# Optimization experiments

Hardware: AMD Instinct MI355X
Metric: run time of the kernel (lower is better)

Reference implementation:

```python
import jax, jax.numpy as jnp
import numpy as np

EPS = 1e-5

def headwise_linear(x, w):
    # x: [B,S,D], w: [NH, DH_out, DH_in] block-diagonal linear per head
    B, S, D = x.shape
    NH, O, DH = w.shape
    xh = x.reshape(B, S, NH, DH)
    return jnp.einsum('bshd,hod->bsho', xh, w).reshape(B, S, NH * O)

def setup_inputs() -> dict:
    key = jax.random.key(0)
    ks = jax.random.split(key, 10)
    B, S, D, NH, K = 8, 4096, 768, 4, 4
    DH = D // NH
    small = (2.0 / (5.0 * D)) ** 0.5  # small_init scale
    return {
        'x': jax.random.normal(ks[0], (B, S, D), jnp.float32),
        'conv_w': jax.random.normal(ks[1], (D, 1, K), jnp.float32) * (1.0 / K ** 0.5),
        'conv_b': jnp.zeros((D,), jnp.float32),
        'w_f': jax.random.normal(ks[2], (NH, DH, DH), jnp.float32) * small,
        'w_i': jax.random.normal(ks[3], (NH, DH, DH), jnp.float32) * small,
        'w_z': jax.random.normal(ks[4], (NH, DH, DH), jnp.float32) * small,
        'w_o': jax.random.normal(ks[5], (NH, DH, DH), jnp.float32) * small,
        'r_kernel': jax.random.normal(ks[6], (NH, DH, 4, DH), jnp.float32) * (1.0 / DH ** 0.5),
        'r_bias': jnp.zeros((4, NH, DH), jnp.float32),
        'gn_weight': jnp.ones((D,), jnp.float32),
    }

def reference(x, conv_w, conv_b, w_f, w_i, w_z, w_o, r_kernel, r_bias, gn_weight):
    B, S, D = x.shape
    NH, DH = r_kernel.shape[0], r_kernel.shape[1]
    K = conv_w.shape[-1]
    # --- causal depthwise conv1d + SiLU ---
    xt = jnp.transpose(x, (0, 2, 1))  # [B,D,S]
    xc = jax.lax.conv_general_dilated(xt, conv_w, (1,), [(K - 1, 0)],
                                      feature_group_count=D)
    x_conv = jax.nn.silu(jnp.transpose(xc + conv_b[None, :, None], (0, 2, 1)))
    # --- headwise gate projections (note: original code feeds fgate->i, igate->f) ---
    gi = headwise_linear(x_conv, w_f)
    gf = headwise_linear(x_conv, w_i)
    gz = headwise_linear(x, w_z)
    go = headwise_linear(x, w_o)
    Wx = jnp.stack([gi, gf, gz, go], axis=2).reshape(B, S, 4, NH, DH)
    Wx = jnp.transpose(Wx, (1, 0, 2, 3, 4))  # [S,B,4,NH,DH]
    # --- sLSTM recurrent scan with exponential gating + stabilizer m ---
    def step(carry, wx_t):
        y, c, n, m = carry  # each [B,NH,DH]
        Ry = jnp.einsum('bhd,hdge->bghe', y, r_kernel)  # [B,4,NH,DH]
        raw = wx_t + Ry + r_bias[None]
        iraw, fraw, zraw, oraw = raw[:, 0], raw[:, 1], raw[:, 2], raw[:, 3]
        logfplusm = m + jax.nn.log_sigmoid(fraw)
        mnew = jnp.maximum(iraw, logfplusm)
        igate = jnp.exp(iraw - mnew)
        fgate = jnp.exp(logfplusm - mnew)
        cnew = fgate * c + igate * jnp.tanh(zraw)
        nnew = fgate * n + igate
        ynew = jax.nn.sigmoid(oraw) * cnew / nnew
        return (ynew, cnew, nnew, mnew), ynew
    init = tuple(jnp.zeros((B, NH, DH), x.dtype) for _ in range(4))
    _, ys = jax.lax.scan(step, init, Wx)  # [S,B,NH,DH]
    y = jnp.transpose(ys, (1, 2, 0, 3))  # [B,NH,S,DH]
    # --- multi-head layer norm (group norm with NH groups over DH) ---
    mean = y.mean(-1, keepdims=True)
    var = y.var(-1, keepdims=True)
    yn = (y - mean) * jax.lax.rsqrt(var + EPS)
    yn = yn * gn_weight.reshape(1, NH, 1, DH)
    return jnp.transpose(yn, (0, 2, 1, 3)).reshape(B, S, NH * DH)
```

## Files before the change

kernel.cpp:

```cpp
#include <hip/hip_runtime.h>
#include <hip/hip_bf16.h>
#include <math.h>

#define B_ 8
#define S_ 4096
#define D_ 768
#define NH_ 4
#define DH_ 192
#define NTOT_ 768

typedef __attribute__((ext_vector_type(8))) short short8;
typedef __attribute__((ext_vector_type(4))) float floatx4;
typedef __attribute__((ext_vector_type(4))) short short4v;
typedef __attribute__((ext_vector_type(4))) unsigned int uint4v;
typedef _Float16 f16;

__device__ __forceinline__ short f2bs(float f) {
  union { float f; unsigned u; } v; v.f = f;
  unsigned r = v.u + 0x7FFFu + ((v.u >> 16) & 1u);
  return (short)(r >> 16);
}
__device__ __forceinline__ float bs2f(unsigned short s) {
  union { unsigned u; float f; } v; v.u = ((unsigned)s) << 16;
  return v.f;
}
__device__ __forceinline__ unsigned packh2(float lo, float hi) {
  union { f16 h[2]; unsigned u; } x;
  x.h[0] = (f16)lo; x.h[1] = (f16)hi;
  return x.u;
}

__device__ __forceinline__ float DOT2(unsigned r, unsigned y, float acc) {
  asm("v_dot2_f32_f16 %0, %1, %2, %0" : "+v"(acc) : "v"(r), "v"(y));
  return acc;
}

template<int CTRL>
__device__ __forceinline__ float qperm(float x) {
  return __int_as_float(__builtin_amdgcn_mov_dpp(__float_as_int(x), CTRL, 0xf, 0xf, true));
}

__global__ __launch_bounds__(256) void wconv_kernel(
    const float* __restrict__ wf, const float* __restrict__ wi,
    const float* __restrict__ wz, const float* __restrict__ wo,
    short* __restrict__ Wbf)
{
  int idx = blockIdx.x * 256 + threadIdx.x;
  int hg = idx / (DH_ * DH_);
  int r  = idx % (DH_ * DH_);
  int h = hg >> 2, g = hg & 3;
  const float* W = (g == 0) ? wf : (g == 1) ? wi : (g == 2) ? wz : wo;
  Wbf[idx] = f2bs(W[(size_t)h * DH_ * DH_ + r]);
}

__global__ __launch_bounds__(256) void conv_silu_kernel(
    const float* __restrict__ x, const float* __restrict__ cw, const float* __restrict__ cb,
    short* __restrict__ xb, short* __restrict__ xcb)
{
  const int b  = blockIdx.x / (S_ / 64);
  const int s0 = (blockIdx.x % (S_ / 64)) * 64;
  const int tid = threadIdx.x;
  float wv[3][4], bias[3], win[3][3];
  for (int j = 0; j < 3; ++j) {
    int d = tid + j * 256;
    for (int k = 0; k < 4; ++k) wv[j][k] = cw[d * 4 + k];
    bias[j] = cb[d];
    for (int p = 0; p < 3; ++p) {
      int s = s0 - 3 + p;
      win[j][p] = (s >= 0) ? x[((size_t)b * S_ + s) * D_ + d] : 0.f;
    }
  }
  for (int i = 0; i < 64; ++i) {
    size_t base = ((size_t)b * S_ + (s0 + i)) * D_;
    for (int j = 0; j < 3; ++j) {
      int d = tid + j * 256;
      float xc = x[base + d];
      float a = bias[j] + win[j][0] * wv[j][0] + win[j][1] * wv[j][1]
                        + win[j][2] * wv[j][2] + xc * wv[j][3];
      float sv = a / (1.f + __expf(-a));
      xb[base + d]  = f2bs(xc);
      xcb[base + d] = f2bs(sv);
      win[j][0] = win[j][1]; win[j][1] = win[j][2]; win[j][2] = xc;
    }
  }
}

__global__ __launch_bounds__(256) void proj_kernel(
    const short* __restrict__ xb, const short* __restrict__ xcb,
    const short* __restrict__ Wbf, const float* __restrict__ rb,
    short* __restrict__ P)
{
  const int hg = blockIdx.y;
  const int h = hg >> 2, g = hg & 3;
  const short* A  = (g < 2) ? xcb : xb;
  const short* Wb = Wbf + (size_t)hg * (DH_ * DH_);
  const int tid = threadIdx.x, w = tid >> 6, l = tid & 63;
  const int l15 = l & 15, lg = l >> 4;
  const int R0 = blockIdx.x * 256 + w * 64;

  float rbv[12];
#pragma unroll
  for (int nt = 0; nt < 12; ++nt)
    rbv[nt] = rb[(g * NH_ + h) * DH_ + l15 + nt * 16];

  for (int mp = 0; mp < 2; ++mp) {
    const int rb0 = R0 + mp * 32;
    floatx4 acc[2][12];
    for (int u = 0; u < 2; ++u)
      for (int nt = 0; nt < 12; ++nt) acc[u][nt] = (floatx4){0.f, 0.f, 0.f, 0.f};
    const short* Ar = A + (size_t)(rb0 + l15) * D_ + h * DH_ + lg * 8;
    const short* Bp = Wb + l15 * DH_ + lg * 8;
    for (int kk = 0; kk < 6; ++kk) {
      short8 a0 = *(const short8*)(Ar + kk * 32);
      short8 a1 = *(const short8*)(Ar + (size_t)16 * D_ + kk * 32);
      for (int nt = 0; nt < 12; ++nt) {
        short8 bf = *(const short8*)(Bp + nt * 16 * DH_ + kk * 32);
        acc[0][nt] = __builtin_amdgcn_mfma_f32_16x16x32_bf16(a0, bf, acc[0][nt], 0, 0, 0);
        acc[1][nt] = __builtin_amdgcn_mfma_f32_16x16x32_bf16(a1, bf, acc[1][nt], 0, 0, 0);
      }
    }
    for (int u = 0; u < 2; ++u) {
      for (int q = 0; q < 4; ++q) {
        int row = rb0 + u * 16 + lg * 4 + q;
        int s = row & (S_ - 1);
        int bb = row >> 12;
        size_t ob = (((size_t)h * B_ + bb) * S_ + s) * NTOT_ + l15 * 4 + g;
        for (int nt = 0; nt < 12; ++nt)
          P[ob + nt * 64] = f2bs(acc[u][nt][q] + rbv[nt]);
      }
    }
  }
}

#define RL_BYTES 147456
#define CHUNK_B  12288
__global__ __launch_bounds__(768)
void scan_kernel(short* P_, const float* __restrict__ rk)
{
  const int bid = blockIdx.x;
  const int h = bid >> 3;
  const int t0 = threadIdx.x;
  const int e = t0 >> 2, q = t0 & 3;

  __shared__ __align__(16) char shbuf[RL_BYTES + 2 * DH_ * 2];
  f16* ybuf = (f16*)(shbuf + RL_BYTES);

  const float* Rh = rk + (size_t)h * (DH_ * NTOT_);

  unsigned Rr[2][24];
#pragma unroll
  for (int j = 0; j < 24; ++j) {
    const int k0 = 48 * q + 2 * j;
#pragma unroll
    for (int g = 0; g < 2; ++g) {
      float v0 = Rh[((size_t)k0 * 4 + g) * DH_ + e];
      float v1 = Rh[((size_t)(k0 + 1) * 4 + g) * DH_ + e];
      Rr[g][j] = packh2(v0, v1);
    }
  }
#pragma unroll
  for (int c = 0; c < 12; ++c) {
    const int gate = 2 + (c >= 6);
    const int m0 = (c % 6) * 4;
    uint4v blk;
#pragma unroll
    for (int j = 0; j < 4; ++j) {
      const int k0 = 48 * q + 2 * (m0 + j);
      blk[j] = packh2(Rh[((size_t)k0 * 4 + gate) * DH_ + e],
                      Rh[((size_t)(k0 + 1) * 4 + gate) * DH_ + e]);
    }
    *(uint4v*)(shbuf + c * CHUNK_B + t0 * 16) = blk;
  }

  if (t0 < DH_) ybuf[t0] = (f16)0.f;

  float c = 0.f, nrm = 0.f, m = 0.f;
  short* Pc = P_ + (size_t)bid * S_ * NTOT_;
  short4v wxc = *(const short4v*)(Pc + e * 4);
  __syncthreads();

  const char* rlz = shbuf + t0 * 16;
  const char* rlo = rlz + 6 * CHUNK_B;

#pragma unroll 1
  for (int t = 0; t < S_; ++t) {
    short4v wxn = {};
    if (t + 1 < S_) wxn = *(const short4v*)(Pc + (size_t)(t + 1) * NTOT_ + e * 4);

    const f16* yb = ybuf + (t & 1) * DH_ + q * 48;
    float a0 = 0.f, a1 = 0.f, a2 = 0.f, a3 = 0.f;
#pragma unroll
    for (int i = 0; i < 6; ++i) {
      uint4v Y = *(const uint4v*)(yb + i * 8);
      uint4v Z = *(const uint4v*)(rlz + i * CHUNK_B);
      uint4v O = *(const uint4v*)(rlo + i * CHUNK_B);
#pragma unroll
      for (int u = 0; u < 4; ++u) {
        const int j = i * 4 + u;
        a0 = DOT2(Rr[0][j], Y[u], a0);
        a1 = DOT2(Rr[1][j], Y[u], a1);
        a2 = DOT2(Z[u], Y[u], a2);
        a3 = DOT2(O[u], Y[u], a3);
      }
    }
    a0 += qperm<0xB1>(a0);  a0 += qperm<0x4E>(a0);
    a1 += qperm<0xB1>(a1);  a1 += qperm<0x4E>(a1);
    a2 += qperm<0xB1>(a2);  a2 += qperm<0x4E>(a2);
    a3 += qperm<0xB1>(a3);  a3 += qperm<0x4E>(a3);

    float ir  = bs2f((unsigned short)wxc[0]) + a0;
    float fr  = bs2f((unsigned short)wxc[1]) + a1;
    float zr  = bs2f((unsigned short)wxc[2]) + a2;
    float orr = bs2f((unsigned short)wxc[3]) + a3;

    float lsf = fminf(fr, 0.f) - __logf(1.f + __expf(-fabsf(fr)));
    float lfm = m + lsf;
    float mnew = fmaxf(ir, lfm);
    float ig = __expf(ir - mnew);
    float fg = __expf(lfm - mnew);
    float e2z = __expf(2.f * zr);
    float tz = 1.f - 2.f * __builtin_amdgcn_rcpf(e2z + 1.f);
    c   = fg * c + ig * tz;
    nrm = fg * nrm + ig;
    m = mnew;
    float sg = __builtin_amdgcn_rcpf(1.f + __expf(-orr));
    float y = sg * c * __builtin_amdgcn_rcpf(nrm);

    f16 yh = (f16)y;
    if (q == 0) {
      ybuf[((t & 1) ^ 1) * DH_ + e] = yh;
      union { f16 hh; short ss; } uv; uv.hh = yh;
      Pc[(size_t)t * NTOT_ + e] = uv.ss;
    }
    wxc = wxn;
    __syncthreads();
  }
}

__global__ __launch_bounds__(256) void gnorm_kernel(
    const short* __restrict__ yws, const float* __restrict__ gnw,
    float* __restrict__ out)
{
  const int row = blockIdx.x * 4 + (threadIdx.x >> 6);
  const int l = threadIdx.x & 63;
  const int h = row >> 15;
  const int b = (row >> 12) & 7;
  const int s = row & (S_ - 1);
  const short* yr = yws + (size_t)row * NTOT_;
  float v[3];
  float su = 0.f, sq = 0.f;
#pragma unroll
  for (int j = 0; j < 3; ++j) {
    unsigned short u = (unsigned short)yr[l + j * 64];
    union { unsigned short u; f16 h; } cv; cv.u = u;
    v[j] = (float)cv.h;
    su += v[j]; sq += v[j] * v[j];
  }
  for (int off = 32; off; off >>= 1) {
    su += __shfl_xor(su, off);
    sq += __shfl_xor(sq, off);
  }
  float mean = su * (1.f / DH_);
  float var = sq * (1.f / DH_) - mean * mean;
  float rs = rsqrtf(var + 1e-5f);
  float* orow = out + ((size_t)b * S_ + s) * D_ + h * DH_;
#pragma unroll
  for (int j = 0; j < 3; ++j)
    orow[l + j * 64] = (v[j] - mean) * rs * gnw[h * DH_ + l + j * 64];
}

extern "C" void kernel_launch(void* const* d_in, const int* in_sizes, int n_in,
                              void* d_out, int out_size, void* d_ws, size_t ws_size,
                              hipStream_t stream) {
  const float* x   = (const float*)d_in[0];
  const float* cw  = (const float*)d_in[1];
  const float* cb  = (const float*)d_in[2];
  const float* wf  = (const float*)d_in[3];
  const float* wi  = (const float*)d_in[4];
  const float* wz  = (const float*)d_in[5];
  const float* wo  = (const float*)d_in[6];
  const float* rk  = (const float*)d_in[7];
  const float* rb  = (const float*)d_in[8];
  const float* gnw = (const float*)d_in[9];
  float* out = (float*)d_out;

  short* P   = (short*)d_ws;
  short* Wbf = (short*)((char*)d_ws + (size_t)201326592);
  short* xb  = (short*)d_out;
  short* xcb = (short*)((char*)d_out + (size_t)50331648);

  wconv_kernel<<<dim3(2304), 256, 0, stream>>>(wf, wi, wz, wo, Wbf);
  conv_silu_kernel<<<dim3(512), 256, 0, stream>>>(x, cw, cb, xb, xcb);
  proj_kernel<<<dim3(128, 16), 256, 0, stream>>>(xb, xcb, Wbf, rb, P);
  scan_kernel<<<dim3(32), 768, 0, stream>>>(P, rk);
  gnorm_kernel<<<dim3(32768), 256, 0, stream>>>(P, gnw, out);
}
```

Before: 4.955 ms.

## Compute recurrent f/z/o gate matvecs with MFMA from register-held weights

The per-step recurrent matvec in the scan kernel moves from fp16 dot2 on packed weights to bf16 MFMA for the f, z and o gates. Those weight fragments now stay in registers rather than being read from a large LDS buffer every step. The input gate still uses dot2 with register weights. MFMA results are exchanged through a small LDS array, which adds a second __syncthreads per timestep, and the y buffer is no longer double-buffered. This removes per-step LDS weight traffic, but wastes MFMA work (all 16 rows are identical), adds a barrier to the serial step, and lowers precision to bf16 for the recurrent weights and state.

```diff
diff --git a/kernel.cpp b/kernel.cpp
--- a/kernel.cpp
+++ b/kernel.cpp
@@ -132,8 +132,6 @@
   }
 }
 
-#define RL_BYTES 147456
-#define CHUNK_B  12288
 __global__ __launch_bounds__(768)
 void scan_kernel(short* P_, const float* __restrict__ rk)
 {
@@ -141,77 +139,77 @@
   const int h = bid >> 3;
   const int t0 = threadIdx.x;
   const int e = t0 >> 2, q = t0 & 3;
-
-  __shared__ __align__(16) char shbuf[RL_BYTES + 2 * DH_ * 2];
-  f16* ybuf = (f16*)(shbuf + RL_BYTES);
+  const int w = t0 >> 6, l = t0 & 63;
+  const int l15 = l & 15, lg = l >> 4;
+
+  __shared__ __align__(16) f16 y_f16[DH_];
+  __shared__ __align__(16) unsigned short y_bf[DH_];
+  __shared__ __align__(16) float raw_lds[3][DH_];
 
   const float* Rh = rk + (size_t)h * (DH_ * NTOT_);
 
-  unsigned Rr[2][24];
+  unsigned Ri[24];
 #pragma unroll
   for (int j = 0; j < 24; ++j) {
     const int k0 = 48 * q + 2 * j;
-#pragma unroll
-    for (int g = 0; g < 2; ++g) {
-      float v0 = Rh[((size_t)k0 * 4 + g) * DH_ + e];
-      float v1 = Rh[((size_t)(k0 + 1) * 4 + g) * DH_ + e];
-      Rr[g][j] = packh2(v0, v1);
-    }
-  }
-#pragma unroll
-  for (int c = 0; c < 12; ++c) {
-    const int gate = 2 + (c >= 6);
-    const int m0 = (c % 6) * 4;
-    uint4v blk;
-#pragma unroll
-    for (int j = 0; j < 4; ++j) {
-      const int k0 = 48 * q + 2 * (m0 + j);
-      blk[j] = packh2(Rh[((size_t)k0 * 4 + gate) * DH_ + e],
-                      Rh[((size_t)(k0 + 1) * 4 + gate) * DH_ + e]);
-    }
-    *(uint4v*)(shbuf + c * CHUNK_B + t0 * 16) = blk;
-  }
-
-  if (t0 < DH_) ybuf[t0] = (f16)0.f;
+    Ri[j] = packh2(Rh[(size_t)k0 * NTOT_ + e], Rh[(size_t)(k0 + 1) * NTOT_ + e]);
+  }
+
+  short8 Bf[3][6];
+#pragma unroll
+  for (int gg = 0; gg < 3; ++gg) {
+#pragma unroll
+    for (int kk = 0; kk < 6; ++kk) {
+      short8 v;
+#pragma unroll
+      for (int j = 0; j < 8; ++j) {
+        const int k = kk * 32 + lg * 8 + j;
+        v[j] = f2bs(Rh[(size_t)k * NTOT_ + (gg + 1) * DH_ + w * 16 + l15]);
+      }
+      Bf[gg][kk] = v;
+    }
+  }
+
+  if (t0 < DH_) { y_f16[t0] = (f16)0.f; y_bf[t0] = 0; }
 
   float c = 0.f, nrm = 0.f, m = 0.f;
   short* Pc = P_ + (size_t)bid * S_ * NTOT_;
   short4v wxc = *(const short4v*)(Pc + e * 4);
   __syncthreads();
 
-  const char* rlz = shbuf + t0 * 16;
-  const char* rlo = rlz + 6 * CHUNK_B;
-
 #pragma unroll 1
   for (int t = 0; t < S_; ++t) {
     short4v wxn = {};
     if (t + 1 < S_) wxn = *(const short4v*)(Pc + (size_t)(t + 1) * NTOT_ + e * 4);
 
-    const f16* yb = ybuf + (t & 1) * DH_ + q * 48;
-    float a0 = 0.f, a1 = 0.f, a2 = 0.f, a3 = 0.f;
-#pragma unroll
-    for (int i = 0; i < 6; ++i) {
-      uint4v Y = *(const uint4v*)(yb + i * 8);
-      uint4v Z = *(const uint4v*)(rlz + i * CHUNK_B);
-      uint4v O = *(const uint4v*)(rlo + i * CHUNK_B);
-#pragma unroll
-      for (int u = 0; u < 4; ++u) {
-        const int j = i * 4 + u;
-        a0 = DOT2(Rr[0][j], Y[u], a0);
-        a1 = DOT2(Rr[1][j], Y[u], a1);
-        a2 = DOT2(Z[u], Y[u], a2);
-        a3 = DOT2(O[u], Y[u], a3);
-      }
+    floatx4 acc0 = (floatx4){0.f,0.f,0.f,0.f};
+    floatx4 acc1 = (floatx4){0.f,0.f,0.f,0.f};
+    floatx4 acc2 = (floatx4){0.f,0.f,0.f,0.f};
+    float a0 = 0.f;
+#pragma unroll
+    for (int kk = 0; kk < 6; ++kk) {
+      short8 A = *(const short8*)((const short*)y_bf + kk * 32 + lg * 8);
+      acc0 = __builtin_amdgcn_mfma_f32_16x16x32_bf16(A, Bf[0][kk], acc0, 0, 0, 0);
+      acc1 = __builtin_amdgcn_mfma_f32_16x16x32_bf16(A, Bf[1][kk], acc1, 0, 0, 0);
+      acc2 = __builtin_amdgcn_mfma_f32_16x16x32_bf16(A, Bf[2][kk], acc2, 0, 0, 0);
+      uint4v Y = *(const uint4v*)((const f16*)y_f16 + q * 48 + kk * 8);
+      a0 = DOT2(Ri[kk * 4 + 0], Y[0], a0);
+      a0 = DOT2(Ri[kk * 4 + 1], Y[1], a0);
+      a0 = DOT2(Ri[kk * 4 + 2], Y[2], a0);
+      a0 = DOT2(Ri[kk * 4 + 3], Y[3], a0);
     }
     a0 += qperm<0xB1>(a0);  a0 += qperm<0x4E>(a0);
-    a1 += qperm<0xB1>(a1);  a1 += qperm<0x4E>(a1);
-    a2 += qperm<0xB1>(a2);  a2 += qperm<0x4E>(a2);
-    a3 += qperm<0xB1>(a3);  a3 += qperm<0x4E>(a3);
+    if (l < 16) {
+      raw_lds[0][w * 16 + l] = acc0[0];
+      raw_lds[1][w * 16 + l] = acc1[0];
+      raw_lds[2][w * 16 + l] = acc2[0];
+    }
+    __syncthreads();
 
     float ir  = bs2f((unsigned short)wxc[0]) + a0;
-    float fr  = bs2f((unsigned short)wxc[1]) + a1;
-    float zr  = bs2f((unsigned short)wxc[2]) + a2;
-    float orr = bs2f((unsigned short)wxc[3]) + a3;
+    float fr  = bs2f((unsigned short)wxc[1]) + raw_lds[0][e];
+    float zr  = bs2f((unsigned short)wxc[2]) + raw_lds[1][e];
+    float orr = bs2f((unsigned short)wxc[3]) + raw_lds[2][e];
 
     float lsf = fminf(fr, 0.f) - __logf(1.f + __expf(-fabsf(fr)));
     float lfm = m + lsf;
@@ -226,9 +224,10 @@
     float sg = __builtin_amdgcn_rcpf(1.f + __expf(-orr));
     float y = sg * c * __builtin_amdgcn_rcpf(nrm);
 
-    f16 yh = (f16)y;
     if (q == 0) {
-      ybuf[((t & 1) ^ 1) * DH_ + e] = yh;
+      f16 yh = (f16)y;
+      y_f16[e] = yh;
+      y_bf[e] = (unsigned short)f2bs(y);
       union { f16 hh; short ss; } uv; uv.hh = yh;
       Pc[(size_t)t * NTOT_ + e] = uv.ss;
     }
```

Measured after the change: 5.687 ms. 1.15x slower.
